# Optimization experiments

Hardware: AMD Instinct MI355X
Metric: run time of the kernel (lower is better)

The kernel has to match this reference:

```python
import jax, jax.numpy as jnp
import numpy as np

IN_CH = 256
SCALES = (128.0, 256.0, 512.0)
RATIOS = (0.5, 1.0, 2.0)
A = len(SCALES) * len(RATIOS)
PRE_NMS_TOPK = 2000
POST_NMS_TOPK = 1000
NMS_IOU = 0.7
MIN_SIZE = 16.0
RPN_BATCH = 256
POS_FRAC = 0.5
BBOX_CLAMP = float(np.log(1000.0 / 16.0))


def conv2d(x, w, b, pad):
    y = jax.lax.conv_general_dilated(x, w, (1, 1), [(pad, pad), (pad, pad)],
                                     dimension_numbers=('NCHW', 'OIHW', 'NCHW'))
    return y + b[None, :, None, None]


def generate_anchors(img_hw, feat_hw):
    H, W = img_hw
    Hf, Wf = feat_hw
    sh, sw = H // Hf, W // Wf
    r = jnp.asarray(RATIOS, jnp.float32)
    s = jnp.asarray(SCALES, jnp.float32)
    hr = jnp.sqrt(r)
    wr = 1.0 / hr
    ws = (wr[:, None] * s[None, :]).reshape(-1)  # [A]
    hs = (hr[:, None] * s[None, :]).reshape(-1)
    base = jnp.stack([-ws, -hs, ws, hs], axis=1) * 0.5  # [A,4] zero-centered
    xs = jnp.arange(Wf, dtype=jnp.float32) * sw
    ys = jnp.arange(Hf, dtype=jnp.float32) * sh
    yy, xx = jnp.meshgrid(ys, xs, indexing='ij')
    shifts = jnp.stack([xx, yy, xx, yy], axis=-1).reshape(-1, 4)  # [Hf*Wf,4]
    return (shifts[:, None, :] + base[None, :, :]).reshape(-1, 4)  # [Hf*Wf*A,4]


def apply_deltas(anchors, deltas):
    aw = anchors[:, 2] - anchors[:, 0]
    ah = anchors[:, 3] - anchors[:, 1]
    acx = anchors[:, 0] + 0.5 * aw
    acy = anchors[:, 1] + 0.5 * ah
    dx, dy = deltas[:, 0], deltas[:, 1]
    dw = jnp.minimum(deltas[:, 2], BBOX_CLAMP)
    dh = jnp.minimum(deltas[:, 3], BBOX_CLAMP)
    cx = dx * aw + acx
    cy = dy * ah + acy
    w = jnp.exp(dw) * aw
    h = jnp.exp(dh) * ah
    return jnp.stack([cx - 0.5 * w, cy - 0.5 * h, cx + 0.5 * w, cy + 0.5 * h], axis=1)


def boxes_to_deltas(boxes, anchors):
    aw = anchors[:, 2] - anchors[:, 0]
    ah = anchors[:, 3] - anchors[:, 1]
    acx = anchors[:, 0] + 0.5 * aw
    acy = anchors[:, 1] + 0.5 * ah
    gw = boxes[:, 2] - boxes[:, 0]
    gh = boxes[:, 3] - boxes[:, 1]
    gcx = boxes[:, 0] + 0.5 * gw
    gcy = boxes[:, 1] + 0.5 * gh
    return jnp.stack([(gcx - acx) / aw, (gcy - acy) / ah,
                      jnp.log(gw / aw), jnp.log(gh / ah)], axis=1)


def iou_matrix(a, b):
    area_a = (a[:, 2] - a[:, 0]) * (a[:, 3] - a[:, 1])
    area_b = (b[:, 2] - b[:, 0]) * (b[:, 3] - b[:, 1])
    lt = jnp.maximum(a[:, None, :2], b[None, :, :2])
    rb = jnp.minimum(a[:, None, 2:], b[None, :, 2:])
    wh = jnp.clip(rb - lt, 0.0)
    inter = wh[..., 0] * wh[..., 1]
    return inter / (area_a[:, None] + area_b[None, :] - inter)


def filter_proposals(proposals, logits):
    k = PRE_NMS_TOPK
    top_scores, idx = jax.lax.top_k(logits, k)
    boxes = proposals[idx]
    probs = jax.nn.sigmoid(top_scores)
    bw = boxes[:, 2] - boxes[:, 0]
    bh = boxes[:, 3] - boxes[:, 1]
    probs = jnp.where((bw >= MIN_SIZE) & (bh >= MIN_SIZE), probs, -jnp.inf)
    order = jnp.argsort(-probs)
    boxes = boxes[order]
    probs = probs[order]
    iou = iou_matrix(boxes, boxes)  # [k,k]
    idxs = jnp.arange(k)

    def body(i, keep):
        suppress = keep[i] & (iou[i] > NMS_IOU) & (idxs > i)
        return keep & ~suppress

    keep = jax.lax.fori_loop(0, k, body, jnp.ones(k, bool))
    kept = jnp.where(keep, probs, -jnp.inf)
    final_scores, fidx = jax.lax.top_k(kept, POST_NMS_TOPK)
    return boxes[fidx], final_scores


def _forward(image, feat_map, gt_boxes, w_rpn, b_rpn, w_reg, b_reg, w_cls, b_cls):
    img_hw = image.shape[-2:]
    feat_hw = feat_map.shape[-2:]
    conv_out = jax.nn.relu(conv2d(feat_map, w_rpn, b_rpn, 1))
    reg = conv2d(conv_out, w_reg, b_reg, 0).transpose(0, 2, 3, 1).reshape(-1, 4)
    cls = conv2d(conv_out, w_cls, b_cls, 0).transpose(0, 2, 3, 1).reshape(-1)
    anchors = generate_anchors(img_hw, feat_hw)  # [N,4]
    proposals = apply_deltas(anchors, jax.lax.stop_gradient(reg))
    H, W = img_hw
    proposals = jnp.stack([jnp.clip(proposals[:, 0], 0.0, W),
                           jnp.clip(proposals[:, 1], 0.0, H),
                           jnp.clip(proposals[:, 2], 0.0, W),
                           jnp.clip(proposals[:, 3], 0.0, H)], axis=1)
    prop_out, score_out = filter_proposals(proposals, jax.lax.stop_gradient(cls))

    # --- target assignment (training path) ---
    gt = gt_boxes[0]  # [M,4]
    iou = iou_matrix(anchors, gt)  # [N,M]
    max_iou = iou.max(axis=1)
    argmax_gt = iou.argmax(axis=1)
    labels = jnp.where(max_iou >= 0.7, 1.0, jnp.where(max_iou < 0.3, 0.0, -1.0))
    best_per_gt = iou.max(axis=0)  # [M]
    force_pos = (iou == best_per_gt[None, :]).any(axis=1)
    labels = jnp.where(force_pos, 1.0, labels)
    matched = gt[argmax_gt]
    tgt_deltas = boxes_to_deltas(matched, anchors)

    # --- deterministic positive/negative sampling (fixed key) ---
    N = labels.shape[0]
    u = jax.random.uniform(jax.random.key(42), (N,))
    pos_cap = int(POS_FRAC * RPN_BATCH)
    pv, pi = jax.lax.top_k(jnp.where(labels == 1.0, u, -jnp.inf), pos_cap)
    pos_valid = pv > -jnp.inf
    pos_mask = jnp.zeros(N, bool).at[pi].set(pos_valid)
    num_pos = pos_valid.sum()
    nv, ni = jax.lax.top_k(jnp.where(labels == 0.0, u, -jnp.inf), RPN_BATCH)
    neg_valid = (nv > -jnp.inf) & (jnp.arange(RPN_BATCH) < (RPN_BATCH - num_pos))
    neg_mask = jnp.zeros(N, bool).at[ni].set(neg_valid)
    samp_mask = pos_mask | neg_mask
    n_samp = samp_mask.sum().astype(jnp.float32)

    # BCE with logits (stable), mean over sampled anchors
    bce = jnp.maximum(cls, 0.0) - cls * labels + jnp.log1p(jnp.exp(-jnp.abs(cls)))
    cls_loss = jnp.sum(jnp.where(samp_mask, bce, 0.0)) / n_samp

    # smooth L1 (beta=1/9), sum over positives / num sampled
    beta = 1.0 / 9.0
    d = reg - tgt_deltas
    ad = jnp.abs(d)
    sl1 = jnp.where(ad < beta, 0.5 * d * d / beta, ad - 0.5 * beta)
    loc_loss = jnp.sum(jnp.where(pos_mask[:, None], sl1, 0.0)) / n_samp

    return prop_out, score_out, cls_loss, loc_loss


def setup_inputs() -> dict:
    key = jax.random.key(0)
    ks = jax.random.split(key, 8)
    image = jax.random.normal(ks[0], (1, 3, 800, 800), jnp.float32)
    feat_map = jax.random.normal(ks[1], (1, IN_CH, 100, 100), jnp.float32)
    cxy = jax.random.uniform(ks[2], (1, 20, 2), minval=100.0, maxval=700.0)
    wh = jax.random.uniform(ks[3], (1, 20, 2), minval=50.0, maxval=300.0)
    gt_boxes = jnp.concatenate([jnp.clip(cxy - 0.5 * wh, 0.0, 800.0),
                                jnp.clip(cxy + 0.5 * wh, 0.0, 800.0)], axis=-1)
    w_rpn = 0.01 * jax.random.normal(ks[4], (IN_CH, IN_CH, 3, 3), jnp.float32)
    b_rpn = jnp.zeros((IN_CH,), jnp.float32)
    w_reg = 0.01 * jax.random.normal(ks[5], (A * 4, IN_CH, 1, 1), jnp.float32)
    b_reg = jnp.zeros((A * 4,), jnp.float32)
    w_cls = 0.01 * jax.random.normal(ks[6], (A, IN_CH, 1, 1), jnp.float32)
    b_cls = jnp.zeros((A,), jnp.float32)
    return dict(image=image, feat_map=feat_map, gt_boxes=gt_boxes,
                w_rpn=w_rpn, b_rpn=b_rpn, w_reg=w_reg, b_reg=b_reg,
                w_cls=w_cls, b_cls=b_cls)


def reference(image, feat_map, gt_boxes, w_rpn, b_rpn, w_reg, b_reg, w_cls, b_cls):
    return _forward(image, feat_map, gt_boxes, w_rpn, b_rpn, w_reg, b_reg, w_cls, b_cls)
```

## Files before the change

kernel.cpp:

```cpp
#include <hip/hip_runtime.h>
#include <cstdint>
#include <cstddef>
#include <math.h>

typedef unsigned int u32;
typedef unsigned long long u64;
typedef unsigned char u8;
typedef signed char i8;
typedef unsigned short u16;

#define NPIX 10000
#define NANCH 90000
#define NGT 20
#define DIVUP(a,b) (((a)+(b)-1)/(b))

static constexpr float BBOX_CLAMP_F = 4.135166556742356f;
static constexpr float BETA_F       = 0.1111111111111111111f;
static constexpr float HALF_BETA_F  = 0.0555555555555555556f;

static constexpr size_t algn(size_t x){ return (x + 255) & ~size_t(255); }
static constexpr size_t OFF_WT   = 0;
static constexpr size_t OFF_W1T  = algn(OFF_WT   + size_t(2304)*256*4);
static constexpr size_t OFF_REG  = algn(OFF_W1T  + size_t(64*48*4)*4);
static constexpr size_t OFF_CLS  = algn(OFF_REG  + size_t(NANCH)*4*4);
static constexpr size_t OFF_PROP = algn(OFF_CLS  + size_t(NANCH)*4);
static constexpr size_t OFF_UB   = algn(OFF_PROP + size_t(NANCH)*4*4);
static constexpr size_t OFF_LAB  = algn(OFF_UB   + size_t(NANCH)*4);
static constexpr size_t OFF_AMX  = algn(OFF_LAB  + NANCH);
static constexpr size_t OFF_BGTP = algn(OFF_AMX  + NANCH);
static constexpr size_t OFF_BGT  = algn(OFF_BGTP + 1280*20*4);
static constexpr size_t OFF_BOXA = algn(OFF_BGT  + 256);
static constexpr size_t OFF_BOX2 = algn(OFF_BOXA + 2048*4*4);
static constexpr size_t OFF_PRB2 = algn(OFF_BOX2 + 2048*4*4);
static constexpr size_t OFF_MASK = algn(OFF_PRB2 + 2048*4);
static constexpr size_t OFF_CAND = algn(OFF_MASK + size_t(2048)*32*8);
static constexpr size_t OFF_POSL = algn(OFF_CAND + 4096*8);
static constexpr size_t OFF_EQN  = algn(OFF_POSL + 4096*4);
static constexpr size_t OFF_KEEP = algn(OFF_EQN  + 1024*8);
static constexpr size_t OFF_Z0   = algn(OFF_KEEP + 32*8);
static constexpr size_t OFF_H0   = OFF_Z0;
static constexpr size_t OFF_H2   = OFF_H0 + 65536*4;
static constexpr size_t OFF_META = OFF_H2 + 65536*4;
static constexpr size_t ZERO_END = OFF_META + 256;
static constexpr int ZERO_WORDS  = int((ZERO_END - OFF_Z0) / 4);

enum { M_CAND_CNT=0, M_POS_CNT, M_EQN_CNT, M_NEED_NEG,
       M_BIN_L_HI, M_CUM_L_HI, M_BIN_N_HI, M_CUM_N_HI,
       M_ACC_CLS, M_ACC_LOC, M_N_SAMP };

__device__ __forceinline__ u32 rotl32(u32 x, int d){ return (x<<d)|(x>>(32-d)); }

__device__ __forceinline__ u32 threefry_bits(u32 i) {
  const u32 ks0 = 0u, ks1 = 42u, ks2 = 0x1BD11BDAu ^ 0u ^ 42u;
  u32 x0 = 0u + ks0, x1 = i + ks1;
  x0+=x1; x1=rotl32(x1,13); x1^=x0;
  x0+=x1; x1=rotl32(x1,15); x1^=x0;
  x0+=x1; x1=rotl32(x1,26); x1^=x0;
  x0+=x1; x1=rotl32(x1, 6); x1^=x0;
  x0+=ks1; x1+=ks2+1u;
  x0+=x1; x1=rotl32(x1,17); x1^=x0;
  x0+=x1; x1=rotl32(x1,29); x1^=x0;
  x0+=x1; x1=rotl32(x1,16); x1^=x0;
  x0+=x1; x1=rotl32(x1,24); x1^=x0;
  x0+=ks2; x1+=ks0+2u;
  x0+=x1; x1=rotl32(x1,13); x1^=x0;
  x0+=x1; x1=rotl32(x1,15); x1^=x0;
  x0+=x1; x1=rotl32(x1,26); x1^=x0;
  x0+=x1; x1=rotl32(x1, 6); x1^=x0;
  x0+=ks0; x1+=ks1+3u;
  x0+=x1; x1=rotl32(x1,17); x1^=x0;
  x0+=x1; x1=rotl32(x1,29); x1^=x0;
  x0+=x1; x1=rotl32(x1,16); x1^=x0;
  x0+=x1; x1=rotl32(x1,24); x1^=x0;
  x0+=ks1; x1+=ks2+4u;
  x0+=x1; x1=rotl32(x1,13); x1^=x0;
  x0+=x1; x1=rotl32(x1,15); x1^=x0;
  x0+=x1; x1=rotl32(x1,26); x1^=x0;
  x0+=x1; x1=rotl32(x1, 6); x1^=x0;
  x0+=ks2; x1+=ks0+5u;
  return x1;
}

__device__ __forceinline__ u32 rand_u_bits(u32 i) {
  u32 b = threefry_bits(i);
  float f = __uint_as_float((b >> 9) | 0x3F800000u) - 1.0f;
  return __float_as_uint(f);
}

__device__ __forceinline__ u32 fkey(float x) {
  u32 u = __float_as_uint(x);
  return (u & 0x80000000u) ? ~u : (u | 0x80000000u);
}

__device__ void bitonic_desc(u64* s, int N, int tid, int nthr) {
  for (int k = 2; k <= N; k <<= 1) {
    for (int j = k >> 1; j > 0; j >>= 1) {
      __syncthreads();
      for (int i = tid; i < N; i += nthr) {
        int ixj = i ^ j;
        if (ixj > i) {
          u64 a = s[i], b = s[ixj];
// ... 62 lines not shown
  float acc = bias;
  #pragma unroll 8
  for (int g = 0; g < 64; ++g) {
    float4 a = f4[g], b = w1T4[g*48 + c];
    acc += a.x*b.x + a.y*b.y + a.z*b.z + a.w*b.w;
  }
  return acc;
}

#pragma clang fp contract(off)

__device__ __forceinline__ void anchor_of(int n, float& a0, float& a1, float& a2, float& a3) {
  int px = n / 9, a = n % 9;
  int y = px / 100, x = px % 100;
  int ri = a / 3, si = a % 3;
  const float R[3] = {0.5f, 1.0f, 2.0f};
  const float S[3] = {128.f, 256.f, 512.f};
  float hr = sqrtf(R[ri]);
  float wr = 1.0f / hr;
  float wsa = wr * S[si], hsa = hr * S[si];
  float sx = (float)x * 8.0f, sy = (float)y * 8.0f;
  a0 = sx + (-wsa) * 0.5f;
  a1 = sy + (-hsa) * 0.5f;
  a2 = sx + wsa * 0.5f;
  a3 = sy + hsa * 0.5f;
}

__device__ __forceinline__ float iou_one(float a0,float a1,float a2,float a3,float aarea,
                                         const float* __restrict__ gt, int g) {
  float g0=gt[g*4+0], g1=gt[g*4+1], g2=gt[g*4+2], g3=gt[g*4+3];
  float garea=(g2-g0)*(g3-g1);
  float ix0=fmaxf(a0,g0), iy0=fmaxf(a1,g1);
  float ix1=fminf(a2,g2), iy1=fminf(a3,g3);
  float iw=fmaxf(ix1-ix0,0.f), ih=fmaxf(iy1-iy0,0.f);
  float inter=iw*ih;
  return inter/(aarea+garea-inter);
}

__device__ __forceinline__ float bce_of(float c, float l) {
  return fmaxf(c,0.f) - c*l + log1pf(expf(-fabsf(c)));
}

__global__ __launch_bounds__(256) void k_conv3(const float* __restrict__ feat,
                                               const float* __restrict__ wT,
                                               const float* __restrict__ bias,
                                               const float* __restrict__ w1T,
                                               const float* __restrict__ b_reg,
                                               const float* __restrict__ b_cls,
                                               const float* __restrict__ gt,
                                               float* __restrict__ reg,
                                               float* __restrict__ cls,
                                               float* __restrict__ prop,
                                               u32* __restrict__ h0,
                                               i8* __restrict__ label,
                                               u8* __restrict__ amax,
                                               u32* __restrict__ ub,
                                               float* __restrict__ bgtp) {
  const int co = threadIdx.x;
  const int y0 = (blockIdx.x / 25) * 2;
  const int x0 = (blockIdx.x % 25) * 4;
  __shared__ __align__(16) float sf[16][4][8];
  __shared__ __align__(16) float sacc[8][256];
  __shared__ float shead[8][48];
  __shared__ float sbias[48];
  __shared__ float sgt[80];
  __shared__ float svm[72][20];
  float acc[2][4];
  #pragma unroll
  for (int r = 0; r < 2; ++r)
    #pragma unroll
    for (int p = 0; p < 4; ++p) acc[r][p] = 0.f;

  for (int cb = 0; cb < 256; cb += 16) {
    __syncthreads();
    #pragma unroll
    for (int e = threadIdx.x; e < 512; e += 256) {
      int ci = e >> 5, rem = e & 31, r = rem >> 3, xx = rem & 7;
      int gy = y0 - 1 + r, gx = x0 - 1 + xx;
      float v = 0.f;
      if ((unsigned)gy < 100u && (unsigned)gx < 100u) v = feat[(cb+ci)*NPIX + gy*100 + gx];
      sf[ci][r][xx] = v;
    }
    __syncthreads();
    float wv0[9], wv1[9];
    {
      const float* wp = wT + (size_t)(cb*9)*256 + co;
      #pragma unroll
      for (int k = 0; k < 9; ++k) wv0[k] = wp[k*256];
    }
    #pragma unroll
    for (int ci = 0; ci < 16; ++ci) {
      float* cur = (ci & 1) ? wv1 : wv0;
      float* nxt = (ci & 1) ? wv0 : wv1;
      if (ci < 15) {
        const float* wp = wT + (size_t)((cb+ci+1)*9)*256 + co;
        #pragma unroll
        for (int k = 0; k < 9; ++k) nxt[k] = wp[k*256];
      }
      #pragma unroll
      for (int ir = 0; ir < 4; ++ir) {
        const float4* rp4 = (const float4*)&sf[ci][ir][0];
        float4 q0 = rp4[0], q1 = rp4[1];
        float rw[6] = {q0.x, q0.y, q0.z, q0.w, q1.x, q1.y};
        #pragma unroll
        for (int ky = 0; ky < 3; ++ky) {
          const int ro = ir - ky;
          if (ro >= 0 && ro < 2) {
            #pragma unroll
            for (int kx = 0; kx < 3; ++kx) {
              const float wvv = cur[ky*3+kx];
              #pragma unroll
              for (int p = 0; p < 4; ++p)
                acc[ro][p] = fmaf(wvv, rw[p+kx], acc[ro][p]);
            }
          }
        }
      }
    }
  }
  float b = bias[co];
  #pragma unroll
  for (int r = 0; r < 2; ++r)
    #pragma unroll
    for (int p = 0; p < 4; ++p)
      sacc[r*4+p][co] = fmaxf(acc[r][p] + b, 0.f);
  if (threadIdx.x < 45)
    sbias[threadIdx.x] = (threadIdx.x < 36) ? b_reg[threadIdx.x] : b_cls[threadIdx.x-36];
  if (threadIdx.x < 80) sgt[threadIdx.x] = gt[threadIdx.x];
  __syncthreads();
  for (int task = threadIdx.x; task < 360; task += 256) {
    int pl = task / 45, c = task % 45;
    float v = conv1_dot_t((const float4*)&sacc[pl][0], (const float4*)w1T, c, sbias[c]);
    shead[pl][c] = v;
    int px = (y0 + (pl >> 2))*100 + x0 + (pl & 3);
    if (c < 36) reg[(size_t)px*36 + c] = v;
    else        cls[(size_t)px*9 + (c-36)] = v;
  }
  __syncthreads();
  if (threadIdx.x < 72) {
    int pl = threadIdx.x / 9, aidx = threadIdx.x % 9;
    int px = (y0 + (pl >> 2))*100 + x0 + (pl & 3);
    int n = px*9 + aidx;
    float a0,a1,a2,a3; anchor_of(n, a0,a1,a2,a3);
    float aw = a2 - a0, ah = a3 - a1;
    float acx = a0 + 0.5f*aw, acy = a1 + 0.5f*ah;
    {
      float dx = shead[pl][aidx*4+0], dy = shead[pl][aidx*4+1];
      float dw = fminf(shead[pl][aidx*4+2], BBOX_CLAMP_F);
      float dh = fminf(shead[pl][aidx*4+3], BBOX_CLAMP_F);
      float lg = shead[pl][36+aidx];
      float cx = dx*aw + acx, cy = dy*ah + acy;
      float w = expf(dw)*aw, h = expf(dh)*ah;
      float p0 = cx - 0.5f*w, p1 = cy - 0.5f*h, p2 = cx + 0.5f*w, p3 = cy + 0.5f*h;
      p0 = fminf(fmaxf(p0, 0.f), 800.f);
      p1 = fminf(fmaxf(p1, 0.f), 800.f);
      p2 = fminf(fmaxf(p2, 0.f), 800.f);
      p3 = fminf(fmaxf(p3, 0.f), 800.f);
      prop[(size_t)n*4+0] = p0; prop[(size_t)n*4+1] = p1;
      prop[(size_t)n*4+2] = p2; prop[(size_t)n*4+3] = p3;
      atomicAdd(&h0[fkey(lg) >> 16], 1u);
    }
    float aarea = (a2-a0)*(a3-a1);
    float best = -1.f; int bg = 0;
    for (int g = 0; g < NGT; ++g) {
      float iou = iou_one(a0,a1,a2,a3,aarea,sgt,g);
      svm[threadIdx.x][g] = iou;
      if (iou > best) { best = iou; bg = g; }
    }
    label[n] = (best >= 0.7f) ? (i8)1 : ((best < 0.3f) ? (i8)0 : (i8)-1);
    amax[n] = (u8)bg;
    ub[n] = rand_u_bits((u32)n);
  }
  __syncthreads();
  if (threadIdx.x < NGT) {
    float m = 0.f;
    for (int r = 0; r < 72; ++r) m = fmaxf(m, svm[r][threadIdx.x]);
    bgtp[(size_t)blockIdx.x*NGT + threadIdx.x] = m;
  }
}

__global__ __launch_bounds__(1024) void k_scan(const u32* __restrict__ h0,
                                               const float* __restrict__ bgtp,
                                               u32* __restrict__ meta,
                                               float* __restrict__ bgt) {
  __shared__ u32 s1[1024], part[256], buf[256], sseg;
  __shared__ float pb[32][20];
  int tid = threadIdx.x;
  {
    u32 s = 0;
    const u32* hp = h0 + tid*64;
    for (int i = 0; i < 64; ++i) s += hp[i];
    s1[tid] = s;
  }
  if (tid < 640) {
    int g = tid % 20, ch = tid / 20;
    int r0 = ch*40, r1 = r0 + 40; if (r1 > 1250) r1 = 1250;
    float m = 0.f;
    for (int r = r0; r < r1; ++r) m = fmaxf(m, bgtp[(size_t)r*NGT + g]);
    pb[ch][g] = m;
  }
  __syncthreads();
  if (tid < 256) part[tid] = s1[tid*4] + s1[tid*4+1] + s1[tid*4+2] + s1[tid*4+3];
  __syncthreads();
  if (tid == 0) {
    u32 cum = 0; int seg = 255;
    for (; seg > 0; --seg) { if (cum + part[seg] >= 2000u) break; cum += part[seg]; }
    sseg = (u32)seg; meta[M_CUM_L_HI] = cum;
  }
  if (tid < 20) {
    float m = 0.f;
    #pragma unroll
    for (int c = 0; c < 32; ++c) m = fmaxf(m, pb[c][tid]);
    bgt[tid] = m;
  }
  __syncthreads();
  if (tid < 256) buf[tid] = h0[sseg*256 + tid];
  __syncthreads();
  if (tid == 0) {
    u32 cum = meta[M_CUM_L_HI]; int bin = (int)sseg*256;
    for (int i = 255; i >= 0; --i) {
      u32 h = buf[i];
      if (cum + h >= 2000u) { bin = (int)sseg*256 + i; break; }
      cum += h;
    }
    meta[M_BIN_L_HI] = (u32)bin;
  }
}

__global__ __launch_bounds__(256) void k_force(const float* __restrict__ cls,
                                               const float* __restrict__ bgt,
                                               const float* __restrict__ gt,
                                               i8* __restrict__ label,
                                               const u32* __restrict__ ub,
                                               u32* __restrict__ meta,
                                               u32* __restrict__ poslist,
                                               u32* __restrict__ h2,
                                               u64* __restrict__ cand) {
  __shared__ float sgt[80], sbgt[20];
  int tid = threadIdx.x;
  if (tid < 80) sgt[tid] = gt[tid];
  if (tid < 20) sbgt[tid] = bgt[tid];
  __syncthreads();
  int n = blockIdx.x*256 + tid;
  bool valid = n < NANCH;
  u32 K = meta[M_BIN_L_HI] << 16;
  bool pos = false, pred = false; u64 ckey = 0;
  if (valid) {
    u32 k = fkey(cls[n]);
    if (k >= K) { pred = true; ckey = ((u64)k << 32) | (u64)(0xFFFFFFFFu - (u32)n); }
    float a0,a1,a2,a3; anchor_of(n, a0,a1,a2,a3);
    float aarea = (a2-a0)*(a3-a1);
    bool force = false;
    for (int g = 0; g < NGT; ++g)
      if (iou_one(a0,a1,a2,a3,aarea,sgt,g) == sbgt[g]) force = true;
    i8 lab = label[n];
    if (force) lab = 1;
    label[n] = lab;
    if (lab == 1) pos = true;
    else if (lab == 0) atomicAdd(&h2[ub[n] >> 16], 1u);
  }
  int slot = wave_append(&meta[M_POS_CNT], pos);
  if (pos && slot >= 0 && slot < 4096) poslist[slot] = (u32)n;
  int cslot = wave_append(&meta[M_CAND_CNT], pred);
  if (pred && cslot >= 0 && cslot < 4096) cand[cslot] = ckey;
}

struct MidSh {
  union {
    struct { u64 ss[4096]; float sprob[2048]; u16 dmap[2048]; } srt;
    struct { u32 s1[1024]; u32 part[256]; u32 buf[256]; } ns;
    struct { u64 ss[4096]; u32 sel[128]; float red[1024]; } ps;
  } u;
  u32 sseg;
};

__global__ __launch_bounds__(1024) void k_mid(const u64* __restrict__ cand,
                                              const float* __restrict__ cls,
                                              const float* __restrict__ prop,
                                              const float* __restrict__ reg,
                                              const float* __restrict__ gt,
                                              const u32* __restrict__ ub,
                                              const u32* __restrict__ poslist,
                                              const u8* __restrict__ amax,
                                              const u32* __restrict__ h2,
                                              u32* __restrict__ meta,
                                              float* __restrict__ boxA,
                                              float* __restrict__ box2k,
                                              float* __restrict__ prob2k) {
  __shared__ MidSh S;
  int tid = threadIdx.x;
  const int lane = tid & 63, wave = tid >> 6;
  if (blockIdx.x == 0) {
    u32 cnt = meta[M_CAND_CNT]; if (cnt > 4096u) cnt = 4096u;
    int N1 = (cnt > 2048u) ? 4096 : 2048;
    for (int i = tid; i < N1; i += 1024) S.u.srt.ss[i] = (i < (int)cnt) ? cand[i] : 0ull;
    bitonic_desc(S.u.srt.ss, N1, tid, 1024);
    for (int i = tid; i < 2000; i += 1024) {
      u32 n = 0xFFFFFFFFu - (u32)S.u.srt.ss[i];
      float b0 = prop[(size_t)n*4+0], b1 = prop[(size_t)n*4+1];
      float b2 = prop[(size_t)n*4+2], b3 = prop[(size_t)n*4+3];
      float logit = cls[n];
      float p = 1.0f / (1.0f + expf(-logit));
      float bw = b2 - b0, bh = b3 - b1;
      if (!(bw >= 16.0f && bh >= 16.0f)) p = -INFINITY;
      boxA[i*4+0] = b0; boxA[i*4+1] = b1; boxA[i*4+2] = b2; boxA[i*4+3] = b3;
      S.u.srt.sprob[i] = p;
    }
    __syncthreads();
    if (wave == 0) {
      u32 nkeep = 0;
      for (int c = 0; c < 32; ++c) {
        int i = c*64 + lane;
        bool k = (i < 2000) && (S.u.srt.sprob[i] > -INFINITY);
        nkeep += (u32)__popcll(__ballot(k));
      }
      u32 rk = 0, rf = 0;
      for (int c = 0; c < 32; ++c) {
        int i = c*64 + lane;
        bool inb = (i < 2000);
        bool k = inb && (S.u.srt.sprob[i] > -INFINITY);
        u64 mk = __ballot(k);
        u64 mf = __ballot(inb && !k);
        if (inb) {
          u64 below = (1ull << lane) - 1ull;
          u32 dst = k ? (rk + (u32)__popcll(mk & below))
                      : (nkeep + rf + (u32)__popcll(mf & below));
          S.u.srt.dmap[dst] = (u16)i;
        }
        rk += (u32)__popcll(mk);
        rf += (u32)__popcll(mf);
      }
    }
    __syncthreads();
    for (int t = tid; t < 2000; t += 1024) {
      u32 src = S.u.srt.dmap[t];
      prob2k[t] = S.u.srt.sprob[src];
      box2k[t*4+0] = boxA[src*4+0]; box2k[t*4+1] = boxA[src*4+1];
      box2k[t*4+2] = boxA[src*4+2]; box2k[t*4+3] = boxA[src*4+3];
    }
  } else if (blockIdx.x == 1) {
    u32 pc = meta[M_POS_CNT]; if (pc > 4096u) pc = 4096u;
    int npos = pc < 128u ? (int)pc : 128;
    u32 need = (u32)(256 - npos);
    if (tid == 0) meta[M_NEED_NEG] = need;
    {
      u32 s = 0;
      const u32* hp = h2 + tid*64;
      for (int i = 0; i < 64; ++i) s += hp[i];
      S.u.ns.s1[tid] = s;
    }
    __syncthreads();
    if (tid < 256) S.u.ns.part[tid] = S.u.ns.s1[tid*4] + S.u.ns.s1[tid*4+1]
                                    + S.u.ns.s1[tid*4+2] + S.u.ns.s1[tid*4+3];
    __syncthreads();
    if (tid == 0) {
      u32 cum = 0; int seg = 255;
      for (; seg > 0; --seg) { if (cum + S.u.ns.part[seg] >= need) break; cum += S.u.ns.part[seg]; }
      S.sseg = (u32)seg; meta[M_CUM_N_HI] = cum;
    }
    __syncthreads();
    if (tid < 256) S.u.ns.buf[tid] = h2[S.sseg*256 + tid];
    __syncthreads();
    if (tid == 0) {
      u32 cum = meta[M_CUM_N_HI]; int bin = (int)S.sseg*256;
      for (int i = 255; i >= 0; --i) {
        u32 h = S.u.ns.buf[i];
        if (cum + h >= need) { bin = (int)S.sseg*256 + i; break; }
        cum += h;
      }
      meta[M_BIN_N_HI] = (u32)bin;
      meta[M_CUM_N_HI] = cum;
    }
  } else {
    u32 m = meta[M_POS_CNT]; if (m > 4096u) m = 4096u;
    int npos = m < 128u ? (int)m : 128;
    if (m > 128u) {
      int N = 256; while (N < (int)m) N <<= 1;
      for (int i = tid; i < N; i += 1024)
        S.u.ps.ss[i] = (i < (int)m)
          ? (((u64)ub[poslist[i]] << 32) | (u64)(0xFFFFFFFFu - poslist[i]))
          : 0ull;
      bitonic_desc(S.u.ps.ss, N, tid, 1024);
      if (tid < 128) S.u.ps.sel[tid] = 0xFFFFFFFFu - (u32)S.u.ps.ss[tid];
    } else {
      if (tid < (int)m) S.u.ps.sel[tid] = poslist[tid];
    }
    __syncthreads();
    float accC = 0.f, accL = 0.f;
    if (tid < npos) {
      int n = (int)S.u.ps.sel[tid];
      float c = cls[n];
      accC = bce_of(c, 1.0f);
      float a0,a1,a2,a3; anchor_of(n, a0,a1,a2,a3);
      float aw = a2-a0, ah = a3-a1;
      float acx = a0 + 0.5f*aw, acy = a1 + 0.5f*ah;
      int g = amax[n];
      float g0 = gt[g*4+0], g1 = gt[g*4+1], g2 = gt[g*4+2], g3 = gt[g*4+3];
      float gw = g2-g0, gh = g3-g1;
      float gcx = g0 + 0.5f*gw, gcy = g1 + 0.5f*gh;
      float t0 = (gcx-acx)/aw, t1 = (gcy-acy)/ah;
      float t2 = logf(gw/aw), t3 = logf(gh/ah);
      float tt[4] = {t0,t1,t2,t3};
      float sl = 0.f;
      for (int j = 0; j < 4; ++j) {
        float d = reg[(size_t)n*4 + j] - tt[j];
        float ad = fabsf(d);
        sl += (ad < BETA_F) ? (((0.5f*d)*d)/BETA_F) : (ad - HALF_BETA_F);
      }
      accL = sl;
    }
    __syncthreads();
    S.u.ps.red[tid] = accC;
    __syncthreads();
    for (int s = 512; s > 0; s >>= 1) {
      if (tid < s) S.u.ps.red[tid] = S.u.ps.red[tid] + S.u.ps.red[tid+s];
      __syncthreads();
    }
    float totC = S.u.ps.red[0];
    __syncthreads();
    S.u.ps.red[tid] = accL;
    __syncthreads();
    for (int s = 512; s > 0; s >>= 1) {
      if (tid < s) S.u.ps.red[tid] = S.u.ps.red[tid] + S.u.ps.red[tid+s];
      __syncthreads();
    }
    if (tid == 0) {
      float* mf = (float*)meta;
      atomicAdd(&mf[M_ACC_CLS], totC);
      atomicAdd(&mf[M_ACC_LOC], S.u.ps.red[0]);
      atomicAdd(&meta[M_N_SAMP], (u32)npos);
    }
  }
}

struct NnSh {
  union {
    struct { float bx0[2000], by0[2000], bx1[2000], by1[2000], bar[2000]; } nms;
    struct { float redf[1024]; u32 redc[1024]; } neg;
  } u;
};

__global__ __launch_bounds__(1024) void k_nn(const float* __restrict__ box2k,
                                             const float* __restrict__ cls,
                                             const i8* __restrict__ label,
                                             const u32* __restrict__ ub,
                                             u32* __restrict__ meta,
                                             u64* __restrict__ eqn,
                                             u64* __restrict__ mask) {
  __shared__ NnSh S;
  int tid = threadIdx.x;
  int lane = tid & 63;
  int wave = tid >> 6;
  if (blockIdx.x < 125) {
    for (int i = tid; i < 2000; i += 1024) {
      float x0 = box2k[i*4+0], y0 = box2k[i*4+1], x1 = box2k[i*4+2], y1 = box2k[i*4+3];
      S.u.nms.bx0[i]=x0; S.u.nms.by0[i]=y0; S.u.nms.bx1[i]=x1; S.u.nms.by1[i]=y1;
      S.u.nms.bar[i] = (x1-x0)*(y1-y0);
    }
    __syncthreads();
    int i = blockIdx.x*16 + wave;
    if (i < 2000) {
      float x0 = S.u.nms.bx0[i], y0 = S.u.nms.by0[i], x1 = S.u.nms.bx1[i], y1 = S.u.nms.by1[i];
      float ai = S.u.nms.bar[i];
      #pragma unroll 4
      for (int w = 0; w < 32; ++w) {
        int j = w*64 + lane;
        bool sup = false;
        if (j < 2000 && j > i) {
          float ix0 = fmaxf(x0, S.u.nms.bx0[j]), iy0 = fmaxf(y0, S.u.nms.by0[j]);
          float ix1 = fminf(x1, S.u.nms.bx1[j]), iy1 = fminf(y1, S.u.nms.by1[j]);
          float iw = fmaxf(ix1-ix0, 0.f), ih = fmaxf(iy1-iy0, 0.f);
          float inter = iw*ih;
          float iou = inter / (ai + S.u.nms.bar[j] - inter);
          sup = iou > 0.7f;
        }
        u64 m = __ballot(sup);
        if (lane == 0) mask[(size_t)i*32 + w] = m;
      }
    }
  } else {
    u32 binN = meta[M_BIN_N_HI];
    int n = (blockIdx.x - 125)*1024 + tid;
    float accC = 0.f; u32 cnt = 0;
    bool inbin = false; u64 key = 0;
    if (n < NANCH && label[n] == 0) {
      u32 u = ub[n];
      u32 hi = u >> 16;
      if (hi > binN) { accC = bce_of(cls[n], 0.0f); cnt = 1; }
      else if (hi == binN) { inbin = true; key = ((u64)(u & 0xFFFFu) << 32) | (u64)(0xFFFFFFFFu - (u32)n); }
    }
    int slot = wave_append(&meta[M_EQN_CNT], inbin);
    if (inbin && slot >= 0 && slot < 1024) eqn[slot] = key;
    S.u.neg.redf[tid] = accC; S.u.neg.redc[tid] = cnt;
    __syncthreads();
    for (int s = 512; s > 0; s >>= 1) {
      if (tid < s) { S.u.neg.redf[tid] = S.u.neg.redf[tid] + S.u.neg.redf[tid+s];
                     S.u.neg.redc[tid] += S.u.neg.redc[tid+s]; }
      __syncthreads();
    }
    if (tid == 0 && (S.u.neg.redc[0] > 0 || S.u.neg.redf[0] != 0.f)) {
      float* mf = (float*)meta;
      atomicAdd(&mf[M_ACC_CLS], S.u.neg.redf[0]);
      atomicAdd(&meta[M_N_SAMP], S.u.neg.redc[0]);
    }
  }
}

__global__ __launch_bounds__(1024) void k_final(const float* __restrict__ cls,
                                                const u64* __restrict__ eqn,
                                                const u64* __restrict__ mask,
                                                const float* __restrict__ box2k,
                                                const float* __restrict__ prob2k,
                                                u32* __restrict__ meta,
                                                u64* __restrict__ keep,
                                                float* __restrict__ out) {
  __shared__ union {
    u64 ss[1024];
    struct { u32 kw32[64]; u64 keptw; u32 rc[64][64]; } nsc;
    struct { u16 srcmap[1000]; int ngood; } fin;
  } sh;
  __shared__ float red[1024];
  int tid = threadIdx.x;
  int lane = tid & 63, wave = tid >> 6;
  u32 m = meta[M_EQN_CNT]; if (m > 1024u) m = 1024u;
  int N2 = 128; while (N2 < (int)m) N2 <<= 1;
  if (tid < N2) sh.ss[tid] = (tid < (int)m) ? eqn[tid] : 0ull;
// ... 82 lines not shown
    for (int c = 0; c < 32 && fill < 1000; ++c) {
      int i = c*64 + lane;
      bool bad = false;
      if (i < 2000) bad = !((((keep[i>>6] >> (i&63)) & 1ull) != 0) && (prob2k[i] > -INFINITY));
      u64 mb = __ballot(bad);
      if (bad) {
        int r = fill + (int)__popcll(mb & ((1ull << lane) - 1ull));
        if (r < 1000) sh.fin.srcmap[r] = (u16)i;
      }
      fill += (int)__popcll(mb);
    }
  }
  __syncthreads();
  int ng = sh.fin.ngood;
  for (int s = tid; s < 1000; s += 1024) {
    int src = sh.fin.srcmap[s];
    out[4000 + s] = (s < ng) ? prob2k[src] : -3.0e38f;
    out[s*4+0] = box2k[src*4+0];
    out[s*4+1] = box2k[src*4+1];
    out[s*4+2] = box2k[src*4+2];
    out[s*4+3] = box2k[src*4+3];
  }
  if (tid == 0) {
    const float* mf = (const float*)meta;
    u32 nsv = meta[M_N_SAMP];
    float nsamp = (nsv > 0u) ? (float)nsv : 1.0f;
    out[5000] = mf[M_ACC_CLS] / nsamp;
    out[5001] = mf[M_ACC_LOC] / nsamp;
  }
}

extern "C" void kernel_launch(void* const* d_in, const int* in_sizes, int n_in,
                              void* d_out, int out_size, void* d_ws, size_t ws_size,
                              hipStream_t stream) {
  const float* feat  = (const float*)d_in[1];
  const float* gt    = (const float*)d_in[2];
  const float* w_rpn = (const float*)d_in[3];
  const float* b_rpn = (const float*)d_in[4];
  const float* w_reg = (const float*)d_in[5];
  const float* b_reg = (const float*)d_in[6];
  const float* w_cls = (const float*)d_in[7];
  const float* b_cls = (const float*)d_in[8];
  float* out = (float*)d_out;
  char* ws = (char*)d_ws;

  float* wT     = (float*)(ws + OFF_WT);
  float* w1T    = (float*)(ws + OFF_W1T);
  float* reg    = (float*)(ws + OFF_REG);
  float* cls    = (float*)(ws + OFF_CLS);
  float* prop   = (float*)(ws + OFF_PROP);
  u32*   ub     = (u32*)  (ws + OFF_UB);
  i8*    label  = (i8*)   (ws + OFF_LAB);
  u8*    amax   = (u8*)   (ws + OFF_AMX);
  float* bgtp   = (float*)(ws + OFF_BGTP);
  float* bgt    = (float*)(ws + OFF_BGT);
  float* boxA   = (float*)(ws + OFF_BOXA);
  float* box2k  = (float*)(ws + OFF_BOX2);
  float* prob2k = (float*)(ws + OFF_PRB2);
  u64*   mask   = (u64*)  (ws + OFF_MASK);
  u64*   cand   = (u64*)  (ws + OFF_CAND);
  u32*   poslist= (u32*)  (ws + OFF_POSL);
  u64*   eqn    = (u64*)  (ws + OFF_EQN);
  u64*   keep   = (u64*)  (ws + OFF_KEEP);
  u32*   h0     = (u32*)  (ws + OFF_H0);
  u32*   h2     = (u32*)  (ws + OFF_H2);
  u32*   meta   = (u32*)  (ws + OFF_META);

  k_init<<<145 + 64, 256, 0, stream>>>(w_rpn, w_reg, w_cls, wT, w1T,
                                       (u32*)(ws + OFF_Z0), ZERO_WORDS);
  k_conv3<<<1250, 256, 0, stream>>>(feat, wT, b_rpn, w1T, b_reg, b_cls, gt,
                                    reg, cls, prop, h0, label, amax, ub, bgtp);
  k_scan<<<1, 1024, 0, stream>>>(h0, bgtp, meta, bgt);
  k_force<<<DIVUP(NANCH,256), 256, 0, stream>>>(cls, bgt, gt, label, ub, meta,
                                                poslist, h2, cand);
  k_mid<<<3, 1024, 0, stream>>>(cand, cls, prop, reg, gt, ub, poslist, amax, h2,
                                meta, boxA, box2k, prob2k);
  k_nn<<<125 + DIVUP(NANCH,1024), 1024, 0, stream>>>(box2k, cls, label, ub, meta,
                                                     eqn, mask);
  k_final<<<1, 1024, 0, stream>>>(cls, eqn, mask, box2k, prob2k, meta, keep, out);
}
```

Baseline: 594.8 us.

## Remove serial scan kernel and split top-k sort across blocks

Drops the single-block k_scan launch. Coarse histogram partials are now accumulated with extra atomics in k_conv3 and k_force, and the per-GT best IoU with atomicMax. k_force now works out the top-2000 threshold bin itself, and candidates are split into strictly-above-bin and in-bin lists so two blocks of k_mid sort smaller arrays in parallel. The keep/filtered compaction moves from k_mid into k_nn, which reads through an index map, removing serial work from k_mid. The cost is one more atomic per anchor and a threshold scan repeated in every k_force block.

```diff
diff --git a/kernel.cpp b/kernel.cpp
--- a/kernel.cpp
+++ b/kernel.cpp
@@ -27,26 +27,29 @@
 static constexpr size_t OFF_UB   = algn(OFF_PROP + size_t(NANCH)*4*4);
 static constexpr size_t OFF_LAB  = algn(OFF_UB   + size_t(NANCH)*4);
 static constexpr size_t OFF_AMX  = algn(OFF_LAB  + NANCH);
-static constexpr size_t OFF_BGTP = algn(OFF_AMX  + NANCH);
-static constexpr size_t OFF_BGT  = algn(OFF_BGTP + 1280*20*4);
-static constexpr size_t OFF_BOXA = algn(OFF_BGT  + 256);
+static constexpr size_t OFF_BOXA = algn(OFF_AMX  + NANCH);
 static constexpr size_t OFF_BOX2 = algn(OFF_BOXA + 2048*4*4);
 static constexpr size_t OFF_PRB2 = algn(OFF_BOX2 + 2048*4*4);
-static constexpr size_t OFF_MASK = algn(OFF_PRB2 + 2048*4);
+static constexpr size_t OFF_SPRB = algn(OFF_PRB2 + 2048*4);
+static constexpr size_t OFF_MASK = algn(OFF_SPRB + 2048*4);
 static constexpr size_t OFF_CAND = algn(OFF_MASK + size_t(2048)*32*8);
-static constexpr size_t OFF_POSL = algn(OFF_CAND + 4096*8);
+static constexpr size_t OFF_CND2 = algn(OFF_CAND + 2048*8);
+static constexpr size_t OFF_POSL = algn(OFF_CND2 + 4096*8);
 static constexpr size_t OFF_EQN  = algn(OFF_POSL + 4096*4);
 static constexpr size_t OFF_KEEP = algn(OFF_EQN  + 1024*8);
 static constexpr size_t OFF_Z0   = algn(OFF_KEEP + 32*8);
 static constexpr size_t OFF_H0   = OFF_Z0;
 static constexpr size_t OFF_H2   = OFF_H0 + 65536*4;
 static constexpr size_t OFF_META = OFF_H2 + 65536*4;
-static constexpr size_t ZERO_END = OFF_META + 256;
+static constexpr size_t OFF_PT0  = OFF_META + 256;
+static constexpr size_t OFF_PT2  = OFF_PT0 + 1024;
+static constexpr size_t ZERO_END = OFF_PT2 + 1024;
 static constexpr int ZERO_WORDS  = int((ZERO_END - OFF_Z0) / 4);
 
 enum { M_CAND_CNT=0, M_POS_CNT, M_EQN_CNT, M_NEED_NEG,
        M_BIN_L_HI, M_CUM_L_HI, M_BIN_N_HI, M_CUM_N_HI,
-       M_ACC_CLS, M_ACC_LOC, M_N_SAMP };
+       M_ACC_CLS, M_ACC_LOC, M_N_SAMP, M_CAND2_CNT,
+       M_BGT=32 };
 
 __device__ __forceinline__ u32 rotl32(u32 x, int d){ return (x<<d)|(x>>(32-d)); }
 
@@ -215,10 +218,11 @@
                                                float* __restrict__ cls,
                                                float* __restrict__ prop,
                                                u32* __restrict__ h0,
+                                               u32* __restrict__ part0,
+                                               u32* __restrict__ bgtu,
                                                i8* __restrict__ label,
                                                u8* __restrict__ amax,
-                                               u32* __restrict__ ub,
-                                               float* __restrict__ bgtp) {
+                                               u32* __restrict__ ub) {
   const int co = threadIdx.x;
   const int y0 = (blockIdx.x / 25) * 2;
   const int x0 = (blockIdx.x % 25) * 4;
@@ -321,7 +325,9 @@
       p3 = fminf(fmaxf(p3, 0.f), 800.f);
       prop[(size_t)n*4+0] = p0; prop[(size_t)n*4+1] = p1;
       prop[(size_t)n*4+2] = p2; prop[(size_t)n*4+3] = p3;
-      atomicAdd(&h0[fkey(lg) >> 16], 1u);
+      u32 k16 = fkey(lg) >> 16;
+      atomicAdd(&h0[k16], 1u);
+      atomicAdd(&part0[k16 >> 8], 1u);
     }
     float aarea = (a2-a0)*(a3-a1);
     float best = -1.f; int bg = 0;
@@ -338,79 +344,59 @@
   if (threadIdx.x < NGT) {
     float m = 0.f;
     for (int r = 0; r < 72; ++r) m = fmaxf(m, svm[r][threadIdx.x]);
-    bgtp[(size_t)blockIdx.x*NGT + threadIdx.x] = m;
-  }
-}
-
-__global__ __launch_bounds__(1024) void k_scan(const u32* __restrict__ h0,
-                                               const float* __restrict__ bgtp,
-                                               u32* __restrict__ meta,
-                                               float* __restrict__ bgt) {
-  __shared__ u32 s1[1024], part[256], buf[256], sseg;
-  __shared__ float pb[32][20];
-  int tid = threadIdx.x;
-  {
-    u32 s = 0;
-    const u32* hp = h0 + tid*64;
-    for (int i = 0; i < 64; ++i) s += hp[i];
-    s1[tid] = s;
-  }
-  if (tid < 640) {
-    int g = tid % 20, ch = tid / 20;
-    int r0 = ch*40, r1 = r0 + 40; if (r1 > 1250) r1 = 1250;
-    float m = 0.f;
-    for (int r = r0; r < r1; ++r) m = fmaxf(m, bgtp[(size_t)r*NGT + g]);
-    pb[ch][g] = m;
-  }
-  __syncthreads();
-  if (tid < 256) part[tid] = s1[tid*4] + s1[tid*4+1] + s1[tid*4+2] + s1[tid*4+3];
-  __syncthreads();
-  if (tid == 0) {
-    u32 cum = 0; int seg = 255;
-    for (; seg > 0; --seg) { if (cum + part[seg] >= 2000u) break; cum += part[seg]; }
-    sseg = (u32)seg; meta[M_CUM_L_HI] = cum;
-  }
-  if (tid < 20) {
-    float m = 0.f;
-    #pragma unroll
-    for (int c = 0; c < 32; ++c) m = fmaxf(m, pb[c][tid]);
-    bgt[tid] = m;
-  }
-  __syncthreads();
-  if (tid < 256) buf[tid] = h0[sseg*256 + tid];
-  __syncthreads();
-  if (tid == 0) {
-    u32 cum = meta[M_CUM_L_HI]; int bin = (int)sseg*256;
-    for (int i = 255; i >= 0; --i) {
-      u32 h = buf[i];
-      if (cum + h >= 2000u) { bin = (int)sseg*256 + i; break; }
-      cum += h;
-    }
-    meta[M_BIN_L_HI] = (u32)bin;
+    atomicMax(&bgtu[threadIdx.x], __float_as_uint(m));
   }
 }
 
 __global__ __launch_bounds__(256) void k_force(const float* __restrict__ cls,
-                                               const float* __restrict__ bgt,
                                                const float* __restrict__ gt,
                                                i8* __restrict__ label,
                                                const u32* __restrict__ ub,
                                                u32* __restrict__ meta,
                                                u32* __restrict__ poslist,
+                                               const u32* __restrict__ h0,
                                                u32* __restrict__ h2,
-                                               u64* __restrict__ cand) {
+                                               const u32* __restrict__ part0,
+                                               u32* __restrict__ part2,
+                                               u64* __restrict__ cand,
+                                               u64* __restrict__ cand2) {
   __shared__ float sgt[80], sbgt[20];
+  __shared__ u32 spart[256], sbuf[256];
+  __shared__ u32 sseg, scum, sbin;
   int tid = threadIdx.x;
   if (tid < 80) sgt[tid] = gt[tid];
-  if (tid < 20) sbgt[tid] = bgt[tid];
-  __syncthreads();
+  if (tid < 20) sbgt[tid] = __uint_as_float(meta[M_BGT + tid]);
+  spart[tid] = part0[tid];
+  __syncthreads();
+  if (tid == 0) {
+    u32 cum = 0; int seg = 255;
+    for (; seg > 0; --seg) { if (cum + spart[seg] >= 2000u) break; cum += spart[seg]; }
+    sseg = (u32)seg; scum = cum;
+  }
+  __syncthreads();
+  sbuf[tid] = h0[sseg*256 + tid];
+  __syncthreads();
+  if (tid == 0) {
+    u32 cum = scum; int bin = (int)sseg*256;
+    for (int i = 255; i >= 0; --i) {
+      u32 h = sbuf[i];
+      if (cum + h >= 2000u) { bin = (int)sseg*256 + i; break; }
+      cum += h;
+    }
+    sbin = (u32)bin;
+  }
+  __syncthreads();
+  u32 bin = sbin;
   int n = blockIdx.x*256 + tid;
   bool valid = n < NANCH;
-  u32 K = meta[M_BIN_L_HI] << 16;
-  bool pos = false, pred = false; u64 ckey = 0;
+  bool pos = false, predA = false, predB = false; u64 ckey = 0;
   if (valid) {
     u32 k = fkey(cls[n]);
-    if (k >= K) { pred = true; ckey = ((u64)k << 32) | (u64)(0xFFFFFFFFu - (u32)n); }
+    u32 hi = k >> 16;
+    if (hi >= bin) {
+      ckey = ((u64)k << 32) | (u64)(0xFFFFFFFFu - (u32)n);
+      if (hi > bin) predA = true; else predB = true;
+    }
     float a0,a1,a2,a3; anchor_of(n, a0,a1,a2,a3);
     float aarea = (a2-a0)*(a3-a1);
     bool force = false;
@@ -420,24 +406,53 @@
     if (force) lab = 1;
     label[n] = lab;
     if (lab == 1) pos = true;
-    else if (lab == 0) atomicAdd(&h2[ub[n] >> 16], 1u);
+    else if (lab == 0) {
+      u32 u = ub[n];
+      atomicAdd(&h2[u >> 16], 1u);
+      atomicAdd(&part2[u >> 24], 1u);
+    }
   }
   int slot = wave_append(&meta[M_POS_CNT], pos);
   if (pos && slot >= 0 && slot < 4096) poslist[slot] = (u32)n;
-  int cslot = wave_append(&meta[M_CAND_CNT], pred);
-  if (pred && cslot >= 0 && cslot < 4096) cand[cslot] = ckey;
+  int aslot = wave_append(&meta[M_CAND_CNT], predA);
+  if (predA && aslot >= 0 && aslot < 2048) cand[aslot] = ckey;
+  int bslot = wave_append(&meta[M_CAND2_CNT], predB);
+  if (predB && bslot >= 0 && bslot < 4096) cand2[bslot] = ckey;
 }
 
 struct MidSh {
   union {
-    struct { u64 ss[4096]; float sprob[2048]; u16 dmap[2048]; } srt;
-    struct { u32 s1[1024]; u32 part[256]; u32 buf[256]; } ns;
+    struct { u64 ss[2048]; } srtA;
+    struct { u64 ss[4096]; } srtB;
+    struct { u32 part[256]; u32 buf[256]; } ns;
     struct { u64 ss[4096]; u32 sel[128]; float red[1024]; } ps;
   } u;
-  u32 sseg;
+  u32 sseg, scum;
 };
 
+__device__ __forceinline__ void mid_gather(const u64* __restrict__ ss, int cnt, int base,
+                                           const float* __restrict__ cls,
+                                           const float* __restrict__ prop,
+                                           float* __restrict__ boxA,
+                                           float* __restrict__ sprobG,
+                                           int tid) {
+  for (int t = tid; t < cnt; t += 1024) {
+    int rank = base + t;
+    if (rank >= 2000) break;
+    u32 n = 0xFFFFFFFFu - (u32)ss[t];
+    float b0 = prop[(size_t)n*4+0], b1 = prop[(size_t)n*4+1];
+    float b2 = prop[(size_t)n*4+2], b3 = prop[(size_t)n*4+3];
+    float logit = cls[n];
+    float p = 1.0f / (1.0f + expf(-logit));
+    float bw = b2 - b0, bh = b3 - b1;
+    if (!(bw >= 16.0f && bh >= 16.0f)) p = -INFINITY;
+    boxA[rank*4+0] = b0; boxA[rank*4+1] = b1; boxA[rank*4+2] = b2; boxA[rank*4+3] = b3;
+    sprobG[rank] = p;
+  }
+}
+
 __global__ __launch_bounds__(1024) void k_mid(const u64* __restrict__ cand,
+                                              const u64* __restrict__ cand2,
                                               const float* __restrict__ cls,
                                               const float* __restrict__ prop,
                                               const float* __restrict__ reg,
@@ -446,86 +461,47 @@
                                               const u32* __restrict__ poslist,
                                               const u8* __restrict__ amax,
                                               const u32* __restrict__ h2,
+                                              const u32* __restrict__ part2,
                                               u32* __restrict__ meta,
                                               float* __restrict__ boxA,
-                                              float* __restrict__ box2k,
-                                              float* __restrict__ prob2k) {
+                                              float* __restrict__ sprobG) {
   __shared__ MidSh S;
   int tid = threadIdx.x;
-  const int lane = tid & 63, wave = tid >> 6;
   if (blockIdx.x == 0) {
-    u32 cnt = meta[M_CAND_CNT]; if (cnt > 4096u) cnt = 4096u;
-    int N1 = (cnt > 2048u) ? 4096 : 2048;
-    for (int i = tid; i < N1; i += 1024) S.u.srt.ss[i] = (i < (int)cnt) ? cand[i] : 0ull;
-    bitonic_desc(S.u.srt.ss, N1, tid, 1024);
-    for (int i = tid; i < 2000; i += 1024) {
-      u32 n = 0xFFFFFFFFu - (u32)S.u.srt.ss[i];
-      float b0 = prop[(size_t)n*4+0], b1 = prop[(size_t)n*4+1];
-      float b2 = prop[(size_t)n*4+2], b3 = prop[(size_t)n*4+3];
-      float logit = cls[n];
-      float p = 1.0f / (1.0f + expf(-logit));
-      float bw = b2 - b0, bh = b3 - b1;
-      if (!(bw >= 16.0f && bh >= 16.0f)) p = -INFINITY;
-      boxA[i*4+0] = b0; boxA[i*4+1] = b1; boxA[i*4+2] = b2; boxA[i*4+3] = b3;
-      S.u.srt.sprob[i] = p;
-    }
-    __syncthreads();
-    if (wave == 0) {
-      u32 nkeep = 0;
-      for (int c = 0; c < 32; ++c) {
-        int i = c*64 + lane;
-        bool k = (i < 2000) && (S.u.srt.sprob[i] > -INFINITY);
-        nkeep += (u32)__popcll(__ballot(k));
-      }
-      u32 rk = 0, rf = 0;
-      for (int c = 0; c < 32; ++c) {
-        int i = c*64 + lane;
-        bool inb = (i < 2000);
-        bool k = inb && (S.u.srt.sprob[i] > -INFINITY);
-        u64 mk = __ballot(k);
-        u64 mf = __ballot(inb && !k);
-        if (inb) {
-          u64 below = (1ull << lane) - 1ull;
-          u32 dst = k ? (rk + (u32)__popcll(mk & below))
-                      : (nkeep + rf + (u32)__popcll(mf & below));
-          S.u.srt.dmap[dst] = (u16)i;
-        }
-        rk += (u32)__popcll(mk);
-        rf += (u32)__popcll(mf);
-      }
-    }
-    __syncthreads();
-    for (int t = tid; t < 2000; t += 1024) {
-      u32 src = S.u.srt.dmap[t];
-      prob2k[t] = S.u.srt.sprob[src];
-      box2k[t*4+0] = boxA[src*4+0]; box2k[t*4+1] = boxA[src*4+1];
-      box2k[t*4+2] = boxA[src*4+2]; box2k[t*4+3] = boxA[src*4+3];
+    u32 c1 = meta[M_CAND_CNT]; if (c1 > 2048u) c1 = 2048u;
+    if (c1 > 0) {
+      int N = 256; while (N < (int)c1) N <<= 1;
+      for (int i = tid; i < N; i += 1024) S.u.srtA.ss[i] = (i < (int)c1) ? cand[i] : 0ull;
+      bitonic_desc(S.u.srtA.ss, N, tid, 1024);
+      mid_gather(S.u.srtA.ss, (int)c1, 0, cls, prop, boxA, sprobG, tid);
+    }
+  } else if (blockIdx.x == 3) {
+    u32 c1 = meta[M_CAND_CNT]; if (c1 > 2048u) c1 = 2048u;
+    u32 c2 = meta[M_CAND2_CNT]; if (c2 > 4096u) c2 = 4096u;
+    int lim = 2000 - (int)c1; if (lim < 0) lim = 0; if (lim > (int)c2) lim = (int)c2;
+    if (c2 > 0 && lim > 0) {
+      int N = 256; while (N < (int)c2) N <<= 1;
+      for (int i = tid; i < N; i += 1024) S.u.srtB.ss[i] = (i < (int)c2) ? cand2[i] : 0ull;
+      bitonic_desc(S.u.srtB.ss, N, tid, 1024);
+      mid_gather(S.u.srtB.ss, lim, (int)c1, cls, prop, boxA, sprobG, tid);
     }
   } else if (blockIdx.x == 1) {
     u32 pc = meta[M_POS_CNT]; if (pc > 4096u) pc = 4096u;
     int npos = pc < 128u ? (int)pc : 128;
     u32 need = (u32)(256 - npos);
     if (tid == 0) meta[M_NEED_NEG] = need;
-    {
-      u32 s = 0;
-      const u32* hp = h2 + tid*64;
-      for (int i = 0; i < 64; ++i) s += hp[i];
-      S.u.ns.s1[tid] = s;
-    }
-    __syncthreads();
-    if (tid < 256) S.u.ns.part[tid] = S.u.ns.s1[tid*4] + S.u.ns.s1[tid*4+1]
-                                    + S.u.ns.s1[tid*4+2] + S.u.ns.s1[tid*4+3];
+    if (tid < 256) S.u.ns.part[tid] = part2[tid];
     __syncthreads();
     if (tid == 0) {
       u32 cum = 0; int seg = 255;
       for (; seg > 0; --seg) { if (cum + S.u.ns.part[seg] >= need) break; cum += S.u.ns.part[seg]; }
-      S.sseg = (u32)seg; meta[M_CUM_N_HI] = cum;
+      S.sseg = (u32)seg; S.scum = cum;
     }
     __syncthreads();
     if (tid < 256) S.u.ns.buf[tid] = h2[S.sseg*256 + tid];
     __syncthreads();
     if (tid == 0) {
-      u32 cum = meta[M_CUM_N_HI]; int bin = (int)S.sseg*256;
+      u32 cum = S.scum; int bin = (int)S.sseg*256;
       for (int i = 255; i >= 0; --i) {
         u32 h = S.u.ns.buf[i];
         if (cum + h >= need) { bin = (int)S.sseg*256 + i; break; }
@@ -598,43 +574,84 @@
 
 struct NnSh {
   union {
-    struct { float bx0[2000], by0[2000], bx1[2000], by1[2000], bar[2000]; } nms;
+    struct { float bx0[2000], by0[2000], bx1[2000], by1[2000], bar[2000], sp[2000];
+             u16 dmap[2000]; } nms;
     struct { float redf[1024]; u32 redc[1024]; } neg;
   } u;
 };
 
-__global__ __launch_bounds__(1024) void k_nn(const float* __restrict__ box2k,
+__global__ __launch_bounds__(1024) void k_nn(const float* __restrict__ boxA,
+                                             const float* __restrict__ sprobG,
                                              const float* __restrict__ cls,
                                              const i8* __restrict__ label,
                                              const u32* __restrict__ ub,
                                              u32* __restrict__ meta,
                                              u64* __restrict__ eqn,
-                                             u64* __restrict__ mask) {
+                                             u64* __restrict__ mask,
+                                             float* __restrict__ box2k,
+                                             float* __restrict__ prob2k) {
   __shared__ NnSh S;
   int tid = threadIdx.x;
   int lane = tid & 63;
   int wave = tid >> 6;
   if (blockIdx.x < 125) {
     for (int i = tid; i < 2000; i += 1024) {
-      float x0 = box2k[i*4+0], y0 = box2k[i*4+1], x1 = box2k[i*4+2], y1 = box2k[i*4+3];
+      float x0 = boxA[i*4+0], y0 = boxA[i*4+1], x1 = boxA[i*4+2], y1 = boxA[i*4+3];
       S.u.nms.bx0[i]=x0; S.u.nms.by0[i]=y0; S.u.nms.bx1[i]=x1; S.u.nms.by1[i]=y1;
       S.u.nms.bar[i] = (x1-x0)*(y1-y0);
-    }
-    __syncthreads();
+      S.u.nms.sp[i] = sprobG[i];
+    }
+    __syncthreads();
+    if (wave == 0) {
+      u32 nkeep = 0;
+      for (int c = 0; c < 32; ++c) {
+        int i = c*64 + lane;
+        bool k = (i < 2000) && (S.u.nms.sp[i] > -INFINITY);
+        nkeep += (u32)__popcll(__ballot(k));
+      }
+      u32 rk = 0, rf = 0;
+      for (int c = 0; c < 32; ++c) {
+        int i = c*64 + lane;
+        bool inb = (i < 2000);
+        bool k = inb && (S.u.nms.sp[i] > -INFINITY);
+        u64 mk = __ballot(k);
+        u64 mf = __ballot(inb && !k);
+        if (inb) {
+          u64 below = (1ull << lane) - 1ull;
+          u32 dst = k ? (rk + (u32)__popcll(mk & below))
+                      : (nkeep + rf + (u32)__popcll(mf & below));
+          S.u.nms.dmap[dst] = (u16)i;
+        }
+        rk += (u32)__popcll(mk);
+        rf += (u32)__popcll(mf);
+      }
+    }
+    __syncthreads();
+    if (blockIdx.x == 0) {
+      for (int t = tid; t < 2000; t += 1024) {
+        u32 s = S.u.nms.dmap[t];
+        prob2k[t] = S.u.nms.sp[s];
+        box2k[t*4+0] = S.u.nms.bx0[s]; box2k[t*4+1] = S.u.nms.by0[s];
+        box2k[t*4+2] = S.u.nms.bx1[s]; box2k[t*4+3] = S.u.nms.by1[s];
+      }
+    }
     int i = blockIdx.x*16 + wave;
     if (i < 2000) {
-      float x0 = S.u.nms.bx0[i], y0 = S.u.nms.by0[i], x1 = S.u.nms.bx1[i], y1 = S.u.nms.by1[i];
-      float ai = S.u.nms.bar[i];
+      u32 di = S.u.nms.dmap[i];
+      float x0 = S.u.nms.bx0[di], y0 = S.u.nms.by0[di];
+      float x1 = S.u.nms.bx1[di], y1 = S.u.nms.by1[di];
+      float ai = S.u.nms.bar[di];
       #pragma unroll 4
       for (int w = 0; w < 32; ++w) {
         int j = w*64 + lane;
         bool sup = false;
         if (j < 2000 && j > i) {
-          float ix0 = fmaxf(x0, S.u.nms.bx0[j]), iy0 = fmaxf(y0, S.u.nms.by0[j]);
-          float ix1 = fminf(x1, S.u.nms.bx1[j]), iy1 = fminf(y1, S.u.nms.by1[j]);
+          u32 dj = S.u.nms.dmap[j];
+          float ix0 = fmaxf(x0, S.u.nms.bx0[dj]), iy0 = fmaxf(y0, S.u.nms.by0[dj]);
+          float ix1 = fminf(x1, S.u.nms.bx1[dj]), iy1 = fminf(y1, S.u.nms.by1[dj]);
           float iw = fmaxf(ix1-ix0, 0.f), ih = fmaxf(iy1-iy0, 0.f);
           float inter = iw*ih;
-          float iou = inter / (ai + S.u.nms.bar[j] - inter);
+          float iou = inter / (ai + S.u.nms.bar[dj] - inter);
           sup = iou > 0.7f;
         }
         u64 m = __ballot(sup);
@@ -823,30 +840,34 @@
   u32*   ub     = (u32*)  (ws + OFF_UB);
   i8*    label  = (i8*)   (ws + OFF_LAB);
   u8*    amax   = (u8*)   (ws + OFF_AMX);
-  float* bgtp   = (float*)(ws + OFF_BGTP);
-  float* bgt    = (float*)(ws + OFF_BGT);
   float* boxA   = (float*)(ws + OFF_BOXA);
   float* box2k  = (float*)(ws + OFF_BOX2);
   float* prob2k = (float*)(ws + OFF_PRB2);
+  float* sprobG = (float*)(ws + OFF_SPRB);
   u64*   mask   = (u64*)  (ws + OFF_MASK);
   u64*   cand   = (u64*)  (ws + OFF_CAND);
+  u64*   cand2  = (u64*)  (ws + OFF_CND2);
   u32*   poslist= (u32*)  (ws + OFF_POSL);
   u64*   eqn    = (u64*)  (ws + OFF_EQN);
   u64*   keep   = (u64*)  (ws + OFF_KEEP);
   u32*   h0     = (u32*)  (ws + OFF_H0);
   u32*   h2     = (u32*)  (ws + OFF_H2);
   u32*   meta   = (u32*)  (ws + OFF_META);
+  u32*   part0  = (u32*)  (ws + OFF_PT0);
+  u32*   part2  = (u32*)  (ws + OFF_PT2);
 
   k_init<<<145 + 64, 256, 0, stream>>>(w_rpn, w_reg, w_cls, wT, w1T,
                                        (u32*)(ws + OFF_Z0), ZERO_WORDS);
   k_conv3<<<1250, 256, 0, stream>>>(feat, wT, b_rpn, w1T, b_reg, b_cls, gt,
-                                    reg, cls, prop, h0, label, amax, ub, bgtp);
-  k_scan<<<1, 1024, 0, stream>>>(h0, bgtp, meta, bgt);
-  k_force<<<DIVUP(NANCH,256), 256, 0, stream>>>(cls, bgt, gt, label, ub, meta,
-                                                poslist, h2, cand);
-  k_mid<<<3, 1024, 0, stream>>>(cand, cls, prop, reg, gt, ub, poslist, amax, h2,
-                                meta, boxA, box2k, prob2k);
-  k_nn<<<125 + DIVUP(NANCH,1024), 1024, 0, stream>>>(box2k, cls, label, ub, meta,
-                                                     eqn, mask);
+                                    reg, cls, prop, h0, part0, meta + M_BGT,
+                                    label, amax, ub);
+  k_force<<<DIVUP(NANCH,256), 256, 0, stream>>>(cls, gt, label, ub, meta,
+                                                poslist, h0, h2, part0, part2,
+                                                cand, cand2);
+  k_mid<<<4, 1024, 0, stream>>>(cand, cand2, cls, prop, reg, gt, ub, poslist,
+                                amax, h2, part2, meta, boxA, sprobG);
+  k_nn<<<125 + DIVUP(NANCH,1024), 1024, 0, stream>>>(boxA, sprobG, cls, label,
+                                                     ub, meta, eqn, mask,
+                                                     box2k, prob2k);
   k_final<<<1, 1024, 0, stream>>>(cls, eqn, mask, box2k, prob2k, meta, keep, out);
 }
```

Result: slower. 1.288 ms (+116.5%).
